# Performance work log

Measured on AMD Instinct MI355X. Metric: run time of the kernel, lower is better.

Reference implementation:

```python
import jax, jax.numpy as jnp
import numpy as np

A = 100000   # batched action space size
V = 500000   # relation vocab
D = 128      # ExperimentSettings.dim
L = 64       # question token count


def setup_inputs() -> dict:
    key = jax.random.key(0)
    ks = jax.random.split(key, 8)
    return {
        "action_ids": jax.random.randint(ks[0], (A,), 0, V),
        "emb_table": jax.random.normal(ks[1], (V, D), dtype=jnp.float32) * 0.1,
        "question_t": jax.random.normal(ks[2], (L, D), dtype=jnp.float32),
        "history_t": jax.random.normal(ks[3], (D,), dtype=jnp.float32),
        "W1": jax.random.normal(ks[4], (D, 2 * D), dtype=jnp.float32) * 0.05,
        "b1": jnp.zeros((D,), dtype=jnp.float32),
        "W2": jax.random.normal(ks[5], (D, D), dtype=jnp.float32) * 0.05,
        "b2": jnp.zeros((D,), dtype=jnp.float32),
    }


def reference(action_ids, emb_table, question_t, history_t, W1, b1, W2, b2):
    # per-action relation embedding lookup (batched over the action space)
    rel = emb_table[action_ids]                              # [A, D]
    # attention over question tokens, keyed by the relation embedding
    att = jnp.einsum("ld,ad->al", question_t, rel)           # [A, L]
    w = jax.nn.softmax(att, axis=-1)
    question = jnp.einsum("al,ld->ad", w, question_t)        # [A, D]
    # Perceptron(dim, dim, 2*dim): MLP on [history; question], dotted with rel
    hist = jnp.broadcast_to(history_t, question.shape)       # [A, D]
    x = jnp.concatenate([hist, question], axis=-1)           # [A, 2D]
    hidden = jax.nn.relu(x @ W1.T + b1)                      # [A, D]
    out = hidden @ W2.T + b2                                 # [A, D]
    scores = jnp.sum(rel * out, axis=-1)                     # [A]
    return jax.nn.softmax(scores, axis=0)
```

## Files before the change

### kernel.cpp

```cpp
#include <hip/hip_runtime.h>
#include <math.h>


#define BA   64
#define NTHR 256
typedef unsigned short ushort_t;
typedef float  f32x4  __attribute__((ext_vector_type(4)));
typedef short  bf16x8 __attribute__((ext_vector_type(8)));

#define WSTRIDE 4352
#define LDS_USH (4 * WSTRIDE)

__device__ __forceinline__ ushort_t f2bf(float f) {
    unsigned int u = __float_as_uint(f);
    return (ushort_t)((u + 0x7fffu + ((u >> 16) & 1u)) >> 16);
}
__device__ __forceinline__ float bf2f(ushort_t h) {
    return __uint_as_float(((unsigned int)h) << 16);
}

__global__ void k_cvt(const float* __restrict__ Qg, const float* __restrict__ W1,
                      const float* __restrict__ W2,
                      const float* __restrict__ hist, const float* __restrict__ b1,
                      ushort_t* __restrict__ Qbf, ushort_t* __restrict__ QTbf,
                      ushort_t* __restrict__ W1bf, ushort_t* __restrict__ W2bf,
                      float* __restrict__ h1)
{
    if (blockIdx.x == 192) {
        const int lane = threadIdx.x & 63;
        const int w    = threadIdx.x >> 6;
        const float h0  = hist[lane];
        const float h64 = hist[64 + lane];
        #pragma unroll 4
        for (int r = 0; r < 32; ++r) {
            const int j = w * 32 + r;
            float p = fmaf(W1[j * 256 + lane], h0, W1[j * 256 + 64 + lane] * h64);
            #pragma unroll
            for (int o = 1; o < 64; o <<= 1) p += __shfl_xor(p, o);
            if (lane == 0) h1[j] = b1[j] + p;
        }
        return;
    }
    const int i = blockIdx.x * 256 + threadIdx.x;
    if (i < 16384) {
        W1bf[i] = f2bf(W1[(i >> 7) * 256 + 128 + (i & 127)]);
    } else if (i < 32768) {
        const int k = i - 16384;
        W2bf[k] = f2bf(W2[k]);
    } else if (i < 40960) {
        const int k = i - 32768;
        Qbf[k] = f2bf(Qg[k]);
    } else {
        const int k = i - 40960;
        const int d = k >> 6, l = k & 63;
        QTbf[k] = f2bf(Qg[l * 128 + d]);
    }
}

__global__ void __launch_bounds__(NTHR, 2)
k_main(const int* __restrict__ action_ids,
       const float* __restrict__ emb,
       const float* __restrict__ b2,
       const float* __restrict__ h1g,
       const ushort_t* __restrict__ Qbf,
       const ushort_t* __restrict__ QTbf,
       const ushort_t* __restrict__ W1bf,
       const ushort_t* __restrict__ W2bf,
       float* __restrict__ scores,
       float* __restrict__ mb,
       float* __restrict__ sb,
       int A)
{
    __shared__ __align__(16) ushort_t L[LDS_USH];
    const int tid  = threadIdx.x;
    const int w    = tid >> 6;
    const int lane = tid & 63;
    const int c    = lane & 15;
    const int g    = lane >> 4;
    ushort_t* RELw = &L[w * WSTRIDE];
    ushort_t* SCRw = &L[w * WSTRIDE + 2176];
    const int a0   = blockIdx.x * BA + 16 * w;

    bf16x8 relA[4];
    {
        const int ga  = a0 + c;
        const int rid = (ga < A) ? action_ids[ga] : 0;
        const float* er = emb + (size_t)rid * 128;
        #pragma unroll
        for (int ks = 0; ks < 4; ++ks) {
            const float4 v0 = *(const float4*)&er[ks * 32 + g * 8];
            const float4 v1 = *(const float4*)&er[ks * 32 + g * 8 + 4];
            union { bf16x8 v; ushort_t u[8]; } p;
            p.u[0] = f2bf(v0.x); p.u[1] = f2bf(v0.y);
            p.u[2] = f2bf(v0.z); p.u[3] = f2bf(v0.w);
            p.u[4] = f2bf(v1.x); p.u[5] = f2bf(v1.y);
            p.u[6] = f2bf(v1.z); p.u[7] = f2bf(v1.w);
            relA[ks] = p.v;
            *(bf16x8*)&RELw[c * 136 + ks * 32 + g * 8] = p.v;
        }
    }

    f32x4 att[4] = {};
    #pragma unroll
    for (int ks = 0; ks < 4; ++ks)
        #pragma unroll
        for (int nt = 0; nt < 4; ++nt) {
            const bf16x8 bfr = *(const bf16x8*)&Qbf[(16*nt + c) * 128 + ks*32 + g*8];
            att[nt] = __builtin_amdgcn_mfma_f32_16x16x32_bf16(relA[ks], bfr, att[nt], 0, 0, 0);
        }

    {
        float m[4] = { -INFINITY, -INFINITY, -INFINITY, -INFINITY };
        #pragma unroll
        for (int nt = 0; nt < 4; ++nt)
            #pragma unroll
            for (int r = 0; r < 4; ++r) m[r] = fmaxf(m[r], att[nt][r]);
        #pragma unroll
        for (int r = 0; r < 4; ++r) {
            m[r] = fmaxf(m[r], __shfl_xor(m[r], 1));
            m[r] = fmaxf(m[r], __shfl_xor(m[r], 2));
            m[r] = fmaxf(m[r], __shfl_xor(m[r], 4));
            m[r] = fmaxf(m[r], __shfl_xor(m[r], 8));
        }
        float s[4] = { 0.f, 0.f, 0.f, 0.f };
        #pragma unroll
        for (int nt = 0; nt < 4; ++nt)
            #pragma unroll
            for (int r = 0; r < 4; ++r) {
                att[nt][r] = __expf(att[nt][r] - m[r]);
                s[r] += att[nt][r];
            }
        #pragma unroll
        for (int r = 0; r < 4; ++r) {
            s[r] += __shfl_xor(s[r], 1);
            s[r] += __shfl_xor(s[r], 2);
            s[r] += __shfl_xor(s[r], 4);
            s[r] += __shfl_xor(s[r], 8);
            s[r] = 1.f / s[r];
        }
        #pragma unroll
        for (int nt = 0; nt < 4; ++nt)
            #pragma unroll
            for (int r = 0; r < 4; ++r)
                SCRw[(4*g + r) * 72 + 16*nt + c] = f2bf(att[nt][r] * s[r]);
    }

    f32x4 qacc[8] = {};
    #pragma unroll
    for (int ks = 0; ks < 2; ++ks) {
        const bf16x8 afr = *(const bf16x8*)&SCRw[c * 72 + ks*32 + g*8];
        #pragma unroll
        for (int nt = 0; nt < 8; ++nt) {
            const bf16x8 bfr = *(const bf16x8*)&QTbf[(16*nt + c) * 64 + ks*32 + g*8];
            qacc[nt] = __builtin_amdgcn_mfma_f32_16x16x32_bf16(afr, bfr, qacc[nt], 0, 0, 0);
        }
    }
    #pragma unroll
    for (int nt = 0; nt < 8; ++nt)
        #pragma unroll
        for (int r = 0; r < 4; ++r)
            SCRw[(4*g + r) * 136 + 16*nt + c] = f2bf(qacc[nt][r]);

    f32x4 hacc[8] = {};
    #pragma unroll
    for (int ks = 0; ks < 4; ++ks) {
        const bf16x8 afr = *(const bf16x8*)&SCRw[c * 136 + ks*32 + g*8];
        #pragma unroll
        for (int nt = 0; nt < 8; ++nt) {
            const bf16x8 bfr = *(const bf16x8*)&W1bf[(16*nt + c) * 128 + ks*32 + g*8];
            hacc[nt] = __builtin_amdgcn_mfma_f32_16x16x32_bf16(afr, bfr, hacc[nt], 0, 0, 0);
        }
    }
    #pragma unroll
    for (int nt = 0; nt < 8; ++nt) {
        const float hb = h1g[16*nt + c];
        #pragma unroll
        for (int r = 0; r < 4; ++r)
            SCRw[(4*g + r) * 136 + 16*nt + c] = f2bf(fmaxf(hacc[nt][r] + hb, 0.f));
    }

    f32x4 oacc[8] = {};
    #pragma unroll
    for (int ks = 0; ks < 4; ++ks) {
        const bf16x8 afr = *(const bf16x8*)&SCRw[c * 136 + ks*32 + g*8];
        #pragma unroll
        for (int nt = 0; nt < 8; ++nt) {
            const bf16x8 bfr = *(const bf16x8*)&W2bf[(16*nt + c) * 128 + ks*32 + g*8];
            oacc[nt] = __builtin_amdgcn_mfma_f32_16x16x32_bf16(afr, bfr, oacc[nt], 0, 0, 0);
        }
    }
    float sacc[4] = { 0.f, 0.f, 0.f, 0.f };
    #pragma unroll
    for (int nt = 0; nt < 8; ++nt) {
        const float bb = b2[16*nt + c];
        #pragma unroll
        for (int r = 0; r < 4; ++r) {
            const float ov = oacc[nt][r] + bb;
            const float rv = bf2f(RELw[(4*g + r) * 136 + 16*nt + c]);
            sacc[r] = fmaf(ov, rv, sacc[r]);
        }
    }
    #pragma unroll
    for (int r = 0; r < 4; ++r) {
        sacc[r] += __shfl_xor(sacc[r], 1);
        sacc[r] += __shfl_xor(sacc[r], 2);
        sacc[r] += __shfl_xor(sacc[r], 4);
        sacc[r] += __shfl_xor(sacc[r], 8);
    }
    if (c == 0) {
        #pragma unroll
        for (int r = 0; r < 4; ++r) {
            const int ga = a0 + 4*g + r;
            if (ga < A) scores[ga] = sacc[r];
        }
    }

    {
        float m = -INFINITY;
        #pragma unroll
        for (int r = 0; r < 4; ++r)
            if (a0 + 4*g + r < A) m = fmaxf(m, sacc[r]);
        m = fmaxf(m, __shfl_xor(m, 16));
        m = fmaxf(m, __shfl_xor(m, 32));
        float es = 0.f;
        #pragma unroll
        for (int r = 0; r < 4; ++r)
            if (a0 + 4*g + r < A) es += __expf(sacc[r] - m);
        es += __shfl_xor(es, 16);
        es += __shfl_xor(es, 32);
        if (lane == 0) {
            const int idx = blockIdx.x * 4 + w;
            mb[idx] = m;
            sb[idx] = es;
        }
    }
}

__global__ void k_combine(const float* __restrict__ mb, const float* __restrict__ sb,
                          int n, float* __restrict__ MS)
{
    __shared__ float red[256];
    const int tid = threadIdx.x;
    float m = -INFINITY;
    for (int i = tid; i < n; i += 256) m = fmaxf(m, mb[i]);
    red[tid] = m; __syncthreads();
    for (int s = 128; s > 0; s >>= 1) {
        if (tid < s) red[tid] = fmaxf(red[tid], red[tid + s]);
        __syncthreads();
    }
    const float M = red[0];
    __syncthreads();
    float sum = 0.f;
    for (int i = tid; i < n; i += 256) sum += sb[i] * __expf(mb[i] - M);
    red[tid] = sum; __syncthreads();
    for (int s = 128; s > 0; s >>= 1) {
        if (tid < s) red[tid] += red[tid + s];
        __syncthreads();
    }
    if (tid == 0) { MS[0] = M; MS[1] = 1.f / red[0]; }
}

__global__ void k_norm(const float* __restrict__ scores, const float* __restrict__ MS,
                       float* __restrict__ out, int A)
{
    const int i = blockIdx.x * blockDim.x + threadIdx.x;
    if (i < A) out[i] = __expf(scores[i] - MS[0]) * MS[1];
}

extern "C" void kernel_launch(void* const* d_in, const int* in_sizes, int n_in,
                              void* d_out, int out_size, void* d_ws, size_t ws_size,
                              hipStream_t stream)
{
    const int*   action_ids = (const int*)  d_in[0];
    const float* emb        = (const float*)d_in[1];
    const float* Qg         = (const float*)d_in[2];
    const float* hist       = (const float*)d_in[3];
    const float* W1         = (const float*)d_in[4];
    const float* b1         = (const float*)d_in[5];
    const float* W2         = (const float*)d_in[6];
    const float* b2         = (const float*)d_in[7];
    float* out = (float*)d_out;
    const int A    = in_sizes[0];
    const int nblk = (A + BA - 1) / BA;
    const int npar = nblk * 4;

    float* ws  = (float*)d_ws;
    float* h1  = ws;
    float* MS  = ws + 128;
    const int nal = (npar + 255) & ~255;
    float* mbp = ws + 256;
    float* sbp = mbp + nal;
    ushort_t* u0   = (ushort_t*)(sbp + nal);
    ushort_t* Qbf  = u0;
    ushort_t* QTbf = u0 + 8192;
    ushort_t* W1bf = u0 + 16384;
    ushort_t* W2bf = u0 + 32768;
    (void)n_in; (void)out_size; (void)ws_size;

    k_cvt<<<193, 256, 0, stream>>>(Qg, W1, W2, hist, b1,
                                   Qbf, QTbf, W1bf, W2bf, h1);
    k_main<<<nblk, NTHR, 0, stream>>>(action_ids, emb, b2, h1,
                                      Qbf, QTbf, W1bf, W2bf,
                                      out, mbp, sbp, A);
    k_combine<<<1, 256, 0, stream>>>(mbp, sbp, npar, MS);
    k_norm<<<(A + 255) / 256, 256, 0, stream>>>(out, MS, out, A);
}
```

Before: 440.6 us.

## Stage shared weight matrices through LDS with register-prefetched double buffering

Instead of each wave reading the Q, Q^T, W1 and W2 bf16 fragments straight from global/L2 for every MFMA, the block cooperatively stages each 64-row half of every weight matrix into a shared padded LDS tile. The next tile is prefetched into registers while the current one is consumed, with block-wide barriers between phases. Launch bounds are raised to three blocks per CU to improve occupancy. This trades redundant global fragment loads for extra __syncthreads barriers and a larger LDS footprint, which may limit concurrency.

```diff
diff --git a/kernel.cpp b/kernel.cpp
--- a/kernel.cpp
+++ b/kernel.cpp
@@ -8,8 +8,10 @@
 typedef float  f32x4  __attribute__((ext_vector_type(4)));
 typedef short  bf16x8 __attribute__((ext_vector_type(8)));
 
-#define WSTRIDE 4352
-#define LDS_USH (4 * WSTRIDE)
+#define BT    0
+#define RELo  9216
+#define SCRo  17920
+#define LDS_USH 26624
 
 __device__ __forceinline__ ushort_t f2bf(float f) {
     unsigned int u = __float_as_uint(f);
@@ -18,6 +20,19 @@
 __device__ __forceinline__ float bf2f(ushort_t h) {
     return __uint_as_float(((unsigned int)h) << 16);
 }
+
+#define ST_LOAD128(SRC, OFF) do { _Pragma("unroll")                           \
+    for (int it = 0; it < 4; ++it) { const int q = tid + 256 * it;            \
+        stg[it] = *(const bf16x8*)&(SRC)[(OFF) + (q >> 4) * 128 + (q & 15) * 8]; } } while (0)
+#define ST_WRITE136() do { _Pragma("unroll")                                  \
+    for (int it = 0; it < 4; ++it) { const int q = tid + 256 * it;            \
+        *(bf16x8*)&L[BT + (q >> 4) * 136 + (q & 15) * 8] = stg[it]; } } while (0)
+#define ST_LOAD64(SRC) do { _Pragma("unroll")                                 \
+    for (int it = 0; it < 4; ++it) { const int q = tid + 256 * it;            \
+        stg[it] = *(const bf16x8*)&(SRC)[(q >> 3) * 64 + (q & 7) * 8]; } } while (0)
+#define ST_WRITE72() do { _Pragma("unroll")                                   \
+    for (int it = 0; it < 4; ++it) { const int q = tid + 256 * it;            \
+        *(bf16x8*)&L[BT + (q >> 3) * 72 + (q & 7) * 8] = stg[it]; } } while (0)
 
 __global__ void k_cvt(const float* __restrict__ Qg, const float* __restrict__ W1,
                       const float* __restrict__ W2,
@@ -57,7 +72,7 @@
     }
 }
 
-__global__ void __launch_bounds__(NTHR, 2)
+__global__ void __launch_bounds__(NTHR, 3)
 k_main(const int* __restrict__ action_ids,
        const float* __restrict__ emb,
        const float* __restrict__ b2,
@@ -77,15 +92,17 @@
     const int lane = tid & 63;
     const int c    = lane & 15;
     const int g    = lane >> 4;
-    ushort_t* RELw = &L[w * WSTRIDE];
-    ushort_t* SCRw = &L[w * WSTRIDE + 2176];
+    ushort_t* RELw = &L[RELo + w * 2176];
+    ushort_t* SCRw = &L[SCRo + w * 2176];
     const int a0   = blockIdx.x * BA + 16 * w;
+    bf16x8 stg[4];
 
     bf16x8 relA[4];
     {
         const int ga  = a0 + c;
         const int rid = (ga < A) ? action_ids[ga] : 0;
         const float* er = emb + (size_t)rid * 128;
+        ST_LOAD128(Qbf, 0);
         #pragma unroll
         for (int ks = 0; ks < 4; ++ks) {
             const float4 v0 = *(const float4*)&er[ks * 32 + g * 8];
@@ -98,14 +115,17 @@
             relA[ks] = p.v;
             *(bf16x8*)&RELw[c * 136 + ks * 32 + g * 8] = p.v;
         }
-    }
+        ST_WRITE136();
+    }
+    __syncthreads();
 
     f32x4 att[4] = {};
+    ST_LOAD64(QTbf);
     #pragma unroll
     for (int ks = 0; ks < 4; ++ks)
         #pragma unroll
         for (int nt = 0; nt < 4; ++nt) {
-            const bf16x8 bfr = *(const bf16x8*)&Qbf[(16*nt + c) * 128 + ks*32 + g*8];
+            const bf16x8 bfr = *(const bf16x8*)&L[BT + (16*nt + c)*136 + ks*32 + g*8];
             att[nt] = __builtin_amdgcn_mfma_f32_16x16x32_bf16(relA[ks], bfr, att[nt], 0, 0, 0);
         }
 
@@ -144,14 +164,18 @@
             for (int r = 0; r < 4; ++r)
                 SCRw[(4*g + r) * 72 + 16*nt + c] = f2bf(att[nt][r] * s[r]);
     }
+    __syncthreads();
+    ST_WRITE72();
+    __syncthreads();
 
     f32x4 qacc[8] = {};
+    ST_LOAD128(W1bf, 0);
     #pragma unroll
     for (int ks = 0; ks < 2; ++ks) {
         const bf16x8 afr = *(const bf16x8*)&SCRw[c * 72 + ks*32 + g*8];
         #pragma unroll
         for (int nt = 0; nt < 8; ++nt) {
-            const bf16x8 bfr = *(const bf16x8*)&QTbf[(16*nt + c) * 64 + ks*32 + g*8];
+            const bf16x8 bfr = *(const bf16x8*)&L[BT + (16*nt + c)*72 + ks*32 + g*8];
             qacc[nt] = __builtin_amdgcn_mfma_f32_16x16x32_bf16(afr, bfr, qacc[nt], 0, 0, 0);
         }
     }
@@ -160,44 +184,95 @@
         #pragma unroll
         for (int r = 0; r < 4; ++r)
             SCRw[(4*g + r) * 136 + 16*nt + c] = f2bf(qacc[nt][r]);
+    __syncthreads();
+    ST_WRITE136();
+    __syncthreads();
 
     f32x4 hacc[8] = {};
+    ST_LOAD128(W1bf, 8192);
     #pragma unroll
     for (int ks = 0; ks < 4; ++ks) {
         const bf16x8 afr = *(const bf16x8*)&SCRw[c * 136 + ks*32 + g*8];
         #pragma unroll
-        for (int nt = 0; nt < 8; ++nt) {
-            const bf16x8 bfr = *(const bf16x8*)&W1bf[(16*nt + c) * 128 + ks*32 + g*8];
+        for (int nt = 0; nt < 4; ++nt) {
+            const bf16x8 bfr = *(const bf16x8*)&L[BT + (16*nt + c)*136 + ks*32 + g*8];
             hacc[nt] = __builtin_amdgcn_mfma_f32_16x16x32_bf16(afr, bfr, hacc[nt], 0, 0, 0);
         }
     }
-    #pragma unroll
-    for (int nt = 0; nt < 8; ++nt) {
-        const float hb = h1g[16*nt + c];
-        #pragma unroll
-        for (int r = 0; r < 4; ++r)
-            SCRw[(4*g + r) * 136 + 16*nt + c] = f2bf(fmaxf(hacc[nt][r] + hb, 0.f));
-    }
-
-    f32x4 oacc[8] = {};
+    __syncthreads();
+    ST_WRITE136();
+    __syncthreads();
+    ST_LOAD128(W2bf, 0);
     #pragma unroll
     for (int ks = 0; ks < 4; ++ks) {
         const bf16x8 afr = *(const bf16x8*)&SCRw[c * 136 + ks*32 + g*8];
         #pragma unroll
-        for (int nt = 0; nt < 8; ++nt) {
-            const bf16x8 bfr = *(const bf16x8*)&W2bf[(16*nt + c) * 128 + ks*32 + g*8];
-            oacc[nt] = __builtin_amdgcn_mfma_f32_16x16x32_bf16(afr, bfr, oacc[nt], 0, 0, 0);
-        }
-    }
+        for (int nt = 0; nt < 4; ++nt) {
+            const bf16x8 bfr = *(const bf16x8*)&L[BT + (16*nt + c)*136 + ks*32 + g*8];
+            hacc[4 + nt] = __builtin_amdgcn_mfma_f32_16x16x32_bf16(afr, bfr, hacc[4 + nt], 0, 0, 0);
+        }
+    }
+    #pragma unroll
+    for (int i = 0; i < 8; ++i) {
+        const int j = (i >> 2) * 64 + (i & 3) * 16 + c;
+        const float hb = h1g[j];
+        #pragma unroll
+        for (int r = 0; r < 4; ++r)
+            SCRw[(4*g + r) * 136 + j] = f2bf(fmaxf(hacc[i][r] + hb, 0.f));
+    }
+    __syncthreads();
+    ST_WRITE136();
+    __syncthreads();
+
     float sacc[4] = { 0.f, 0.f, 0.f, 0.f };
-    #pragma unroll
-    for (int nt = 0; nt < 8; ++nt) {
-        const float bb = b2[16*nt + c];
-        #pragma unroll
-        for (int r = 0; r < 4; ++r) {
-            const float ov = oacc[nt][r] + bb;
-            const float rv = bf2f(RELw[(4*g + r) * 136 + 16*nt + c]);
-            sacc[r] = fmaf(ov, rv, sacc[r]);
+    {
+        f32x4 oacc[4] = {};
+        ST_LOAD128(W2bf, 8192);
+        #pragma unroll
+        for (int ks = 0; ks < 4; ++ks) {
+            const bf16x8 afr = *(const bf16x8*)&SCRw[c * 136 + ks*32 + g*8];
+            #pragma unroll
+            for (int nt = 0; nt < 4; ++nt) {
+                const bf16x8 bfr = *(const bf16x8*)&L[BT + (16*nt + c)*136 + ks*32 + g*8];
+                oacc[nt] = __builtin_amdgcn_mfma_f32_16x16x32_bf16(afr, bfr, oacc[nt], 0, 0, 0);
+            }
+        }
+        #pragma unroll
+        for (int nt = 0; nt < 4; ++nt) {
+            const int d = 16*nt + c;
+            const float bb = b2[d];
+            #pragma unroll
+            for (int r = 0; r < 4; ++r) {
+                const float ov = oacc[nt][r] + bb;
+                const float rv = bf2f(RELw[(4*g + r) * 136 + d]);
+                sacc[r] = fmaf(ov, rv, sacc[r]);
+            }
+        }
+    }
+    __syncthreads();
+    ST_WRITE136();
+    __syncthreads();
+    {
+        f32x4 oacc[4] = {};
+        #pragma unroll
+        for (int ks = 0; ks < 4; ++ks) {
+            const bf16x8 afr = *(const bf16x8*)&SCRw[c * 136 + ks*32 + g*8];
+            #pragma unroll
+            for (int nt = 0; nt < 4; ++nt) {
+                const bf16x8 bfr = *(const bf16x8*)&L[BT + (16*nt + c)*136 + ks*32 + g*8];
+                oacc[nt] = __builtin_amdgcn_mfma_f32_16x16x32_bf16(afr, bfr, oacc[nt], 0, 0, 0);
+            }
+        }
+        #pragma unroll
+        for (int nt = 0; nt < 4; ++nt) {
+            const int d = 64 + 16*nt + c;
+            const float bb = b2[d];
+            #pragma unroll
+            for (int r = 0; r < 4; ++r) {
+                const float ov = oacc[nt][r] + bb;
+                const float rv = bf2f(RELw[(4*g + r) * 136 + d]);
+                sacc[r] = fmaf(ov, rv, sacc[r]);
+            }
         }
     }
     #pragma unroll
```

Result: faster. 373.2 us (-15.3%).
